# Kernel optimization log

Measured on AMD Instinct MI355X. Metric: run time of the kernel, lower is better.

The kernel has to match this reference:

```python
import jax, jax.numpy as jnp
import numpy as np

B, T, F_IN = 256, 168, 128
H = 512            # encoder hidden per direction; decoder hidden = 2H
OUT = 1
L_OUT = 48
SCALE = 0.05


def _lstm_scan(x, Wih, Whh, b, h0, c0):
    # x: [T, B, F]; PyTorch LSTM gate order i, f, g, o
    def step(carry, xt):
        h, c = carry
        g = xt @ Wih.T + h @ Whh.T + b
        i, f, gg, o = jnp.split(g, 4, axis=-1)
        c = jax.nn.sigmoid(f) * c + jax.nn.sigmoid(i) * jnp.tanh(gg)
        h = jax.nn.sigmoid(o) * jnp.tanh(c)
        return (h, c), h
    (hT, cT), ys = jax.lax.scan(step, (h0, c0), x)
    return ys, hT, cT


def setup_inputs() -> dict:
    key = jax.random.key(0)
    ks = jax.random.split(key, 16)
    r = lambda k, shp: (jax.random.normal(k, shp, dtype=jnp.float32) * SCALE)
    return {
        "input_seq": jax.random.normal(ks[0], (B, T, F_IN), dtype=jnp.float32),
        "enc_Wih_f": r(ks[1], (4 * H, F_IN)),
        "enc_Whh_f": r(ks[2], (4 * H, H)),
        "enc_bih_f": r(ks[3], (4 * H,)),
        "enc_bhh_f": r(ks[4], (4 * H,)),
        "enc_Wih_b": r(ks[5], (4 * H, F_IN)),
        "enc_Whh_b": r(ks[6], (4 * H, H)),
        "enc_bih_b": r(ks[7], (4 * H,)),
        "enc_bhh_b": r(ks[8], (4 * H,)),
        "dec_Wih": r(ks[9], (4 * 2 * H, OUT)),
        "dec_Whh": r(ks[10], (4 * 2 * H, 2 * H)),
        "dec_bih": r(ks[11], (4 * 2 * H,)),
        "dec_bhh": r(ks[12], (4 * 2 * H,)),
        "fc_W": r(ks[13], (OUT, 2 * H)),
        "fc_b": r(ks[14], (OUT,)),
        "output_length": L_OUT,
    }


def reference(input_seq, enc_Wih_f, enc_Whh_f, enc_bih_f, enc_bhh_f,
              enc_Wih_b, enc_Whh_b, enc_bih_b, enc_bhh_b,
              dec_Wih, dec_Whh, dec_bih, dec_bhh, fc_W, fc_b, output_length):
    b = input_seq.shape[0]
    h = enc_Whh_f.shape[1]
    x = jnp.transpose(input_seq, (1, 0, 2))  # [T, B, F]
    h0 = jnp.zeros((b, h), input_seq.dtype)
    c0 = jnp.zeros((b, h), input_seq.dtype)
    # bidirectional encoder (final hidden/cell only are used downstream)
    _, hf, cf = _lstm_scan(x, enc_Wih_f, enc_Whh_f, enc_bih_f + enc_bhh_f, h0, c0)
    _, hb, cb = _lstm_scan(x[::-1], enc_Wih_b, enc_Whh_b, enc_bih_b + enc_bhh_b, h0, c0)
    # _cat_hidden: concat fwd/bwd states along feature dim -> decoder init state [B, 2H]
    hd = jnp.concatenate([hf, hb], axis=-1)
    cd = jnp.concatenate([cf, cb], axis=-1)
    bd = dec_bih + dec_bhh
    x0 = jnp.zeros((b, fc_W.shape[0]), input_seq.dtype)  # initial decoder input = zeros

    def dec_step(carry, _):
        hh, cc, xt = carry
        g = xt @ dec_Wih.T + hh @ dec_Whh.T + bd
        i, f, gg, o = jnp.split(g, 4, axis=-1)
        cc = jax.nn.sigmoid(f) * cc + jax.nn.sigmoid(i) * jnp.tanh(gg)
        hh = jax.nn.sigmoid(o) * jnp.tanh(cc)
        pred = hh @ fc_W.T + fc_b  # [B, OUT]
        return (hh, cc, pred), pred

    _, preds = jax.lax.scan(dec_step, (hd, cd, x0), None, length=output_length)
    # [L, B, OUT] -> [B, L, OUT] -> squeeze(dim=2) with OUT==1 -> [B, L]
    return jnp.transpose(preds, (1, 0, 2)).squeeze(2)
```

## Files before the change

kernel.cpp:

```cpp
#include <hip/hip_runtime.h>


constexpr int B_ = 256, T_ = 168, F_ = 128, H_ = 512, L_ = 48;
constexpr int KE = F_ + H_;
constexpr int HD = 1024;
constexpr int GE = 4 * H_;
constexpr int EPAD = KE + 8;
constexpr int DPAD = HD + 8;

constexpr int FL256_IDX  = 0;
constexpr int CLAIM_IDX  = 256;
constexpr int ENCF_IDX   = 768;
constexpr int DECF_IDX   = 1280;
constexpr int CLAIM2_IDX = 2048;
constexpr int FL2_IDX    = 2560;

constexpr size_t OFF_SYNC = 0;
constexpr size_t OFF_WCF = 16384;
constexpr size_t OFF_WCB = OFF_WCF + (size_t)GE * KE * 2;
constexpr size_t OFF_PP  = OFF_WCB + (size_t)GE * KE * 2;
constexpr size_t OFF_BF  = OFF_PP  + (size_t)8 * 2 * 64 * 32 * 4;
constexpr size_t OFF_BB  = OFF_BF  + (size_t)GE * 4;
constexpr size_t OFF_XH  = OFF_BB  + (size_t)GE * 4;
constexpr size_t OFF_HE  = OFF_XH  + (size_t)T_ * B_ * F_ * 2;
constexpr size_t OFF_HDD = OFF_HE  + (size_t)2 * 2 * B_ * H_ * 2;
constexpr size_t OFF_CD  = OFF_HDD + (size_t)2 * B_ * HD * 2;

using h8 = __attribute__((ext_vector_type(8))) _Float16;
using f4 = __attribute__((ext_vector_type(4))) float;
using u4 = __attribute__((ext_vector_type(4))) unsigned;

#define DEV static __device__ __forceinline__

DEV float sigm(float x)  { return __fdividef(1.f, 1.f + __expf(-x)); }
DEV float tanh_(float x) { return 1.f - __fdividef(2.f, __expf(2.f * x) + 1.f); }

DEV h8 as_h8(f4 v) { union { f4 f; h8 h; } u; u.f = v; return u.h; }

DEV void astore_u64(void* p, unsigned long long v) {
  __hip_atomic_store((unsigned long long*)p, v, __ATOMIC_RELAXED,
                     __HIP_MEMORY_SCOPE_AGENT);
}
DEV void astore_u32(void* p, unsigned v) {
  __hip_atomic_store((unsigned*)p, v, __ATOMIC_RELAXED, __HIP_MEMORY_SCOPE_AGENT);
}
DEV unsigned aload_u32(const void* p) {
  return __hip_atomic_load((const unsigned*)p, __ATOMIC_RELAXED,
                           __HIP_MEMORY_SCOPE_AGENT);
}
DEV float aload_f32(const void* p) {
  return __hip_atomic_load((const float*)p, __ATOMIC_RELAXED,
                           __HIP_MEMORY_SCOPE_AGENT);
}
DEV void astore_f32(void* p, float v) {
  __hip_atomic_store((float*)p, v, __ATOMIC_RELAXED, __HIP_MEMORY_SCOPE_AGENT);
}
DEV void astore_u16(void* p, _Float16 v) {
  union { _Float16 h; unsigned short s; } u; u.h = v;
  __hip_atomic_store((unsigned short*)p, u.s, __ATOMIC_RELAXED,
                     __HIP_MEMORY_SCOPE_AGENT);
}
DEV void vm_drain() { asm volatile("s_waitcnt vmcnt(0)" ::: "memory"); }

template<bool DEEP>
DEV void ld16(const _Float16* p, f4* A) {
#define L16(FL) asm volatile( \
    "global_load_dwordx4 %0,  %16, off" FL "\n\t" \
    "global_load_dwordx4 %1,  %16, off offset:64" FL "\n\t" \
    "global_load_dwordx4 %2,  %16, off offset:128" FL "\n\t" \
    "global_load_dwordx4 %3,  %16, off offset:192" FL "\n\t" \
    "global_load_dwordx4 %4,  %16, off offset:256" FL "\n\t" \
    "global_load_dwordx4 %5,  %16, off offset:320" FL "\n\t" \
    "global_load_dwordx4 %6,  %16, off offset:384" FL "\n\t" \
    "global_load_dwordx4 %7,  %16, off offset:448" FL "\n\t" \
    "global_load_dwordx4 %8,  %16, off offset:512" FL "\n\t" \
    "global_load_dwordx4 %9,  %16, off offset:576" FL "\n\t" \
    "global_load_dwordx4 %10, %16, off offset:640" FL "\n\t" \
    "global_load_dwordx4 %11, %16, off offset:704" FL "\n\t" \
    "global_load_dwordx4 %12, %16, off offset:768" FL "\n\t" \
    "global_load_dwordx4 %13, %16, off offset:832" FL "\n\t" \
    "global_load_dwordx4 %14, %16, off offset:896" FL "\n\t" \
    "global_load_dwordx4 %15, %16, off offset:960" FL "\n\t" \
    "s_waitcnt vmcnt(0)" \
    : "=&v"(A[0]),"=&v"(A[1]),"=&v"(A[2]),"=&v"(A[3]),"=&v"(A[4]),"=&v"(A[5]), \
      "=&v"(A[6]),"=&v"(A[7]),"=&v"(A[8]),"=&v"(A[9]),"=&v"(A[10]),"=&v"(A[11]), \
      "=&v"(A[12]),"=&v"(A[13]),"=&v"(A[14]),"=&v"(A[15]) \
    : "v"(p) : "memory")
  if constexpr (DEEP) { L16(" sc0 sc1"); } else { L16(" sc0"); }
#undef L16
}

template<bool DEEP>
DEV void ld32(const _Float16* p, f4* A) {
#define L32(FL) asm volatile( \
    "global_load_dwordx4 %0,  %32, off" FL "\n\t" \
    "global_load_dwordx4 %1,  %32, off offset:64" FL "\n\t" \
    "global_load_dwordx4 %2,  %32, off offset:128" FL "\n\t" \
    "global_load_dwordx4 %3,  %32, off offset:192" FL "\n\t" \
    "global_load_dwordx4 %4,  %32, off offset:256" FL "\n\t" \
    "global_load_dwordx4 %5,  %32, off offset:320" FL "\n\t" \
    "global_load_dwordx4 %6,  %32, off offset:384" FL "\n\t" \
    "global_load_dwordx4 %7,  %32, off offset:448" FL "\n\t" \
    "global_load_dwordx4 %8,  %32, off offset:512" FL "\n\t" \
    "global_load_dwordx4 %9,  %32, off offset:576" FL "\n\t" \
    "global_load_dwordx4 %10, %32, off offset:640" FL "\n\t" \
    "global_load_dwordx4 %11, %32, off offset:704" FL "\n\t" \
    "global_load_dwordx4 %12, %32, off offset:768" FL "\n\t" \
    "global_load_dwordx4 %13, %32, off offset:832" FL "\n\t" \
    "global_load_dwordx4 %14, %32, off offset:896" FL "\n\t" \
    "global_load_dwordx4 %15, %32, off offset:960" FL "\n\t" \
    "global_load_dwordx4 %16, %32, off offset:1024" FL "\n\t" \
    "global_load_dwordx4 %17, %32, off offset:1088" FL "\n\t" \
    "global_load_dwordx4 %18, %32, off offset:1152" FL "\n\t" \
    "global_load_dwordx4 %19, %32, off offset:1216" FL "\n\t" \
    "global_load_dwordx4 %20, %32, off offset:1280" FL "\n\t" \
    "global_load_dwordx4 %21, %32, off offset:1344" FL "\n\t" \
    "global_load_dwordx4 %22, %32, off offset:1408" FL "\n\t" \
    "global_load_dwordx4 %23, %32, off offset:1472" FL "\n\t" \
    "global_load_dwordx4 %24, %32, off offset:1536" FL "\n\t" \
    "global_load_dwordx4 %25, %32, off offset:1600" FL "\n\t" \
    "global_load_dwordx4 %26, %32, off offset:1664" FL "\n\t" \
    "global_load_dwordx4 %27, %32, off offset:1728" FL "\n\t" \
    "global_load_dwordx4 %28, %32, off offset:1792" FL "\n\t" \
    "global_load_dwordx4 %29, %32, off offset:1856" FL "\n\t" \
    "global_load_dwordx4 %30, %32, off offset:1920" FL "\n\t" \
    "global_load_dwordx4 %31, %32, off offset:1984" FL "\n\t" \
    "s_waitcnt vmcnt(0)" \
    : "=&v"(A[0]),"=&v"(A[1]),"=&v"(A[2]),"=&v"(A[3]),"=&v"(A[4]),"=&v"(A[5]), \
      "=&v"(A[6]),"=&v"(A[7]),"=&v"(A[8]),"=&v"(A[9]),"=&v"(A[10]),"=&v"(A[11]), \
      "=&v"(A[12]),"=&v"(A[13]),"=&v"(A[14]),"=&v"(A[15]),"=&v"(A[16]),"=&v"(A[17]), \
      "=&v"(A[18]),"=&v"(A[19]),"=&v"(A[20]),"=&v"(A[21]),"=&v"(A[22]),"=&v"(A[23]), \
      "=&v"(A[24]),"=&v"(A[25]),"=&v"(A[26]),"=&v"(A[27]),"=&v"(A[28]),"=&v"(A[29]), \
      "=&v"(A[30]),"=&v"(A[31]) \
    : "v"(p) : "memory")
  if constexpr (DEEP) { L32(" sc0 sc1"); } else { L32(" sc0"); }
#undef L32
}

DEV void ld32s(const float* p, float* v) {
  asm volatile(
    "global_load_dword %0,  %32, off sc0 sc1\n\t"
    "global_load_dword %1,  %32, off offset:128 sc0 sc1\n\t"
    "global_load_dword %2,  %32, off offset:256 sc0 sc1\n\t"
    "global_load_dword %3,  %32, off offset:384 sc0 sc1\n\t"
    "global_load_dword %4,  %32, off offset:512 sc0 sc1\n\t"
    "global_load_dword %5,  %32, off offset:640 sc0 sc1\n\t"
    "global_load_dword %6,  %32, off offset:768 sc0 sc1\n\t"
    "global_load_dword %7,  %32, off offset:896 sc0 sc1\n\t"
    "global_load_dword %8,  %32, off offset:1024 sc0 sc1\n\t"
    "global_load_dword %9,  %32, off offset:1152 sc0 sc1\n\t"
    "global_load_dword %10, %32, off offset:1280 sc0 sc1\n\t"
    "global_load_dword %11, %32, off offset:1408 sc0 sc1\n\t"
    "global_load_dword %12, %32, off offset:1536 sc0 sc1\n\t"
    "global_load_dword %13, %32, off offset:1664 sc0 sc1\n\t"
    "global_load_dword %14, %32, off offset:1792 sc0 sc1\n\t"
    "global_load_dword %15, %32, off offset:1920 sc0 sc1\n\t"
    "global_load_dword %16, %32, off offset:2048 sc0 sc1\n\t"
    "global_load_dword %17, %32, off offset:2176 sc0 sc1\n\t"
    "global_load_dword %18, %32, off offset:2304 sc0 sc1\n\t"
    "global_load_dword %19, %32, off offset:2432 sc0 sc1\n\t"
    "global_load_dword %20, %32, off offset:2560 sc0 sc1\n\t"
    "global_load_dword %21, %32, off offset:2688 sc0 sc1\n\t"
    "global_load_dword %22, %32, off offset:2816 sc0 sc1\n\t"
    "global_load_dword %23, %32, off offset:2944 sc0 sc1\n\t"
    "global_load_dword %24, %32, off offset:3072 sc0 sc1\n\t"
    "global_load_dword %25, %32, off offset:3200 sc0 sc1\n\t"
    "global_load_dword %26, %32, off offset:3328 sc0 sc1\n\t"
    "global_load_dword %27, %32, off offset:3456 sc0 sc1\n\t"
    "global_load_dword %28, %32, off offset:3584 sc0 sc1\n\t"
    "global_load_dword %29, %32, off offset:3712 sc0 sc1\n\t"
    "global_load_dword %30, %32, off offset:3840 sc0 sc1\n\t"
    "global_load_dword %31, %32, off offset:3968 sc0 sc1\n\t"
    "s_waitcnt vmcnt(0)"
    : "=&v"(v[0]),"=&v"(v[1]),"=&v"(v[2]),"=&v"(v[3]),"=&v"(v[4]),"=&v"(v[5]),
      "=&v"(v[6]),"=&v"(v[7]),"=&v"(v[8]),"=&v"(v[9]),"=&v"(v[10]),"=&v"(v[11]),
      "=&v"(v[12]),"=&v"(v[13]),"=&v"(v[14]),"=&v"(v[15]),"=&v"(v[16]),"=&v"(v[17]),
      "=&v"(v[18]),"=&v"(v[19]),"=&v"(v[20]),"=&v"(v[21]),"=&v"(v[22]),"=&v"(v[23]),
      "=&v"(v[24]),"=&v"(v[25]),"=&v"(v[26]),"=&v"(v[27]),"=&v"(v[28]),"=&v"(v[29]),
      "=&v"(v[30]),"=&v"(v[31])
    : "v"(p) : "memory");
}

DEV unsigned pollflag(const unsigned* p, bool deep) {
  unsigned v;
  if (deep)
    asm volatile("global_load_dword %0, %1, off sc0 sc1\n\t"
                 "s_waitcnt vmcnt(0)" : "=&v"(v) : "v"(p) : "memory");
  else
    asm volatile("global_load_dword %0, %1, off sc0\n\t"
                 "s_waitcnt vmcnt(0)" : "=&v"(v) : "v"(p) : "memory");
  return v;
}
DEV void wait_ge(const unsigned* p, unsigned target, bool deep, int cap) {
  for (int it = 0; it < cap; ++it) {
    unsigned v = pollflag(p, deep);
    if (__ballot(v >= target) == ~0ull) return;
  }
}

DEV void gsync(unsigned* fl, int bi, unsigned phase, int tid) {
  vm_drain();
  __syncthreads();
  if (tid == 0) astore_u32(fl + bi, phase);
  if (tid < 64) {
    const unsigned* p = fl + tid * 4;
    for (int it = 0; it < (1 << 20); ++it) {
      u4 v;
      asm volatile("global_load_dwordx4 %0, %1, off sc0 sc1\n\t"
                   "s_waitcnt vmcnt(0)" : "=&v"(v) : "v"(p) : "memory");
      unsigned a = v[0] < v[1] ? v[0] : v[1];
      unsigned b = v[2] < v[3] ? v[2] : v[3];
      if (__ballot((a < b ? a : b) >= phase) == ~0ull) break;
    }
  }
  __syncthreads();
  asm volatile("" ::: "memory");
}

__global__ void prep_misc(const float* bihF, const float* bhhF,
                          const float* bihB, const float* bhhB, char* ws) {
  int i = blockIdx.x * blockDim.x + threadIdx.x;
  if (i < 2048) astore_u64(ws + (size_t)i * 8, 0ull);
  if (i < GE) {
    ((float*)(ws + OFF_BF))[i] = bihF[i] + bhhF[i];
    ((float*)(ws + OFF_BB))[i] = bihB[i] + bhhB[i];
  }
  if (i < 2 * 2 * B_ * H_ / 4) astore_u64((char*)ws + OFF_HE + (size_t)i * 8, 0ull);
}

__global__ void conv_encw(const float* WihF, const float* WhhF,
                          const float* WihB, const float* WhhB, char* ws) {
  int i = blockIdx.x * blockDim.x + threadIdx.x;
  if (i >= GE * KE) return;
  int r = i / KE, k = i - r * KE;
  float vF = (k < F_) ? WihF[r * F_ + k] : WhhF[r * H_ + (k - F_)];
  float vB = (k < F_) ? WihB[r * F_ + k] : WhhB[r * H_ + (k - F_)];
  ((_Float16*)(ws + OFF_WCF))[i] = (_Float16)vF;
  ((_Float16*)(ws + OFF_WCB))[i] = (_Float16)vB;
}

__global__ void conv_x(const float* x, char* ws) {
  int i = blockIdx.x * blockDim.x + threadIdx.x;
  if (i >= T_ * B_ * F_) return;
  int f = i & 127, b = (i >> 7) & 255, t = i >> 15;
  ((_Float16*)(ws + OFF_XH))[i] = (_Float16)x[((size_t)b * T_ + t) * F_ + f];
}

template<bool LOCAL>
DEV void encoder_phase(int dir, int chunk, int slice,
                       int tid, int wave, int quad, int col, int lane,
                       char* ws, _Float16* lds, _Float16 (*htile)[16]) {
  const _Float16* Wenc  = (const _Float16*)(ws + (dir ? OFF_WCB : OFF_WCF));
  const float*    biasE = (const float*)(ws + (dir ? OFF_BB : OFF_BF));
  const _Float16* Xh    = (const _Float16*)(ws + OFF_XH);
  _Float16* hE = (_Float16*)(ws + OFF_HE);
  _Float16* hD = (_Float16*)(ws + OFF_HDD);
  float*    cD = (float*)(ws + OFF_CD);
  unsigned* encf = (unsigned*)ws + ENCF_IDX + (dir * 4 + chunk) * 64;

  const int j0 = slice * 16;
  const int mb = chunk * 64;

  for (int it = 0; it < 20; ++it) {
    int idx = it * 256 + tid;
    int n = idx / 80, e = idx - n * 80;
    int g = n >> 4, u = n & 15;
    *((h8*)(lds + n * EPAD) + e) =
        *((const h8*)(Wenc + (size_t)(g * H_ + j0 + u) * KE) + e);
  }
  float breg[4];
#pragma unroll
  for (int g = 0; g < 4; ++g) breg[g] = biasE[g * H_ + j0 + col];
  float cst[4] = {0.f, 0.f, 0.f, 0.f};
  __syncthreads();

  h8 Bf[4][16];
#pragma unroll
  for (int g = 0; g < 4; ++g)
#pragma unroll
    for (int kk = 0; kk < 16; ++kk)
      Bf[g][kk] = *((const h8*)(lds + (g * 16 + col) * EPAD + F_) + kk * 4 + quad);

  const int arow = mb + wave * 16 + col;
  const int mrow = mb + wave * 16 + quad * 4;

  for (int t = 0; t < T_; ++t) {
    const int par = t & 1;
    const int tx  = dir ? (T_ - 1 - t) : t;
    f4 z = {0.f, 0.f, 0.f, 0.f};
    f4 acc[4] = {z, z, z, z};

    const h8* xr = (const h8*)(Xh + ((size_t)tx * B_ + arow) * F_);
#pragma unroll
    for (int kk = 0; kk < 4; ++kk) {
      h8 a = xr[kk * 4 + quad];
#pragma unroll
      for (int g = 0; g < 4; ++g) {
        h8 b = *((const h8*)(lds + (g * 16 + col) * EPAD) + kk * 4 + quad);
        acc[g] = __builtin_amdgcn_mfma_f32_16x16x32_f16(a, b, acc[g], 0, 0, 0);
      }
    }
    if (t > 0)
      wait_ge(encf + (lane & 31), (unsigned)t, !LOCAL, 1 << 16);
    f4 A[16];
    ld16<!LOCAL>(hE + ((size_t)(par * 2 + dir) * B_ + arow) * H_ + quad * 8, A);
#pragma unroll
    for (int kk = 0; kk < 16; ++kk) {
      h8 a = as_h8(A[kk]);
#pragma unroll
      for (int g = 0; g < 4; ++g)
        acc[g] = __builtin_amdgcn_mfma_f32_16x16x32_f16(a, Bf[g][kk], acc[g], 0, 0, 0);
    }

#pragma unroll
    for (int r = 0; r < 4; ++r) {
      float gi = acc[0][r] + breg[0];
      float gf = acc[1][r] + breg[1];
      float gg = acc[2][r] + breg[2];
      float go = acc[3][r] + breg[3];
      float c = sigm(gf) * cst[r] + sigm(gi) * tanh_(gg);
      cst[r] = c;
      float h = sigm(go) * tanh_(c);
      htile[wave * 16 + quad * 4 + r][col] = (_Float16)h;
      if (t == T_ - 1)
        astore_f32(&cD[(size_t)(mrow + r) * HD + dir * H_ + j0 + col], c);
    }
    __syncthreads();
    if (tid < 128) {
      int row = tid >> 1, half = tid & 1;
      const unsigned long long* src =
          (const unsigned long long*)&htile[row][half * 8];
      if (t < T_ - 1) {
        _Float16* dst = hE + ((size_t)((par ^ 1) * 2 + dir) * B_ + mb + row) * H_ +
                        j0 + half * 8;
        if (LOCAL) {
          ((unsigned long long*)dst)[0] = src[0];
          ((unsigned long long*)(dst + 4))[0] = src[1];
        } else {
          astore_u64(dst, src[0]);
          astore_u64(dst + 4, src[1]);
        }
      } else {
        _Float16* dst = hD + (size_t)(mb + row) * HD + dir * H_ + j0 + half * 8;
        astore_u64(dst, src[0]);
        astore_u64(dst + 4, src[1]);
      }
    }
    vm_drain();
    __syncthreads();
    if (tid == 0 && t < T_ - 1) {
      if (LOCAL) *(volatile unsigned*)(encf + slice) = (unsigned)(t + 1);
      else       astore_u32(encf + slice, (unsigned)(t + 1));
    }
  }
}

DEV void decoder_phase(int xcd, int rank, int tid, int wave, int quad, int col,
                       int lane, const float* dWih, const float* dWhh,
                       const float* dbih, const float* dbhh, const float* fcW,
                       const float* fcb, float* out, char* ws, _Float16* lds,
                       float* predbuf) {
  _Float16* hdd = (_Float16*)(ws + OFF_HDD);
  float* cD = (float*)(ws + OFF_CD);
  float* PP = (float*)(ws + OFF_PP) + (size_t)xcd * 2 * 64 * 32;
  unsigned* decf = (unsigned*)ws + DECF_IDX + xcd * 64;

  const int j0b = rank * 32;
  const int R0  = xcd * 32;
  const int m   = wave & 1;
  const int uh  = wave >> 1;
  const int unit = j0b + uh * 16 + col;
  const int arow = R0 + m * 16 + col;
  const int mrow = R0 + m * 16 + quad * 4;

  for (int it = 0; it < 64; ++it) {
    int idx = it * 256 + tid;
    int n = idx >> 8, c = idx & 255;
    int srow = (n >> 5) * HD + j0b + (n & 31);
    f4 w = *((const f4*)(dWhh + (size_t)srow * HD + c * 4));
    union { _Float16 h[4]; unsigned long long q; } u2;
#pragma unroll
    for (int i2 = 0; i2 < 4; ++i2) u2.h[i2] = (_Float16)w[i2];
    *(unsigned long long*)(lds + n * DPAD + c * 4) = u2.q;
  }
  h8 Bf[2][32];
#pragma unroll
  for (int gg = 0; gg < 2; ++gg)
#pragma unroll
    for (int kk = 0; kk < 32; ++kk) {
      const float* src = dWhh + (size_t)((2 + gg) * HD + unit) * HD + kk * 32 + quad * 8;
      f4 w0 = *((const f4*)src);
      f4 w1 = *((const f4*)(src + 4));
      union { _Float16 h[8]; h8 v; } u3;
#pragma unroll
      for (int i2 = 0; i2 < 4; ++i2) {
        u3.h[i2]     = (_Float16)w0[i2];
        u3.h[4 + i2] = (_Float16)w1[i2];
      }
      Bf[gg][kk] = u3.v;
    }
  float breg[4], wreg[4];
#pragma unroll
  for (int g = 0; g < 4; ++g) {
    breg[g] = dbih[g * HD + unit] + dbhh[g * HD + unit];
    wreg[g] = dWih[g * HD + unit];
  }
  const float fcw = fcW[unit];
  const float fb  = fcb[0];
  float cst[4];
#pragma unroll
  for (int r = 0; r < 4; ++r)
    cst[r] = aload_f32(cD + (size_t)(mrow + r) * HD + unit);
  __syncthreads();

  for (int l = 0; l <= L_; ++l) {
    float predv = 0.f;
    if (l > 0) {
      wait_ge(decf + (lane & 31), (unsigned)l, true, 1 << 16);
      const float* PPr = PP + (size_t)((l - 1) & 1) * 64 * 32;
      int row = lane & 31, halfsel = lane >> 5;
      const float* pb = PPr + (size_t)(halfsel * 32) * 32 + row;
      float pv[32], s = 0.f;
      ld32s(pb, pv);
#pragma unroll
      for (int j = 0; j < 32; ++j) s += pv[j];
      s += __shfl_xor(s, 32);
      predv = s + fb;
      if (rank == 0 && wave == 0 && lane < 32)
        predbuf[(l - 1) * 32 + lane] = predv;
    }
    if (l == L_) break;
    const int par = l & 1;

    f4 A[32];
    ld32<true>(hdd + ((size_t)par * B_ + arow) * HD + quad * 8, A);

    f4 z = {0.f, 0.f, 0.f, 0.f};
    f4 acc[4] = {z, z, z, z};
#pragma unroll
    for (int kk = 0; kk < 32; ++kk) {
      h8 a = as_h8(A[kk]);
      h8 b0 = *((const h8*)(lds + (0 * 32 + uh * 16 + col) * DPAD) + kk * 4 + quad);
      h8 b1 = *((const h8*)(lds + (1 * 32 + uh * 16 + col) * DPAD) + kk * 4 + quad);
      acc[0] = __builtin_amdgcn_mfma_f32_16x16x32_f16(a, b0, acc[0], 0, 0, 0);
      acc[1] = __builtin_amdgcn_mfma_f32_16x16x32_f16(a, b1, acc[1], 0, 0, 0);
      acc[2] = __builtin_amdgcn_mfma_f32_16x16x32_f16(a, Bf[0][kk], acc[2], 0, 0, 0);
      acc[3] = __builtin_amdgcn_mfma_f32_16x16x32_f16(a, Bf[1][kk], acc[3], 0, 0, 0);
    }

    float pr[4], sum[4];
#pragma unroll
    for (int r = 0; r < 4; ++r)
      pr[r] = (l > 0) ? __shfl(predv, m * 16 + quad * 4 + r) : 0.f;
#pragma unroll
    for (int r = 0; r < 4; ++r) {
      float gi = acc[0][r] + breg[0] + pr[r] * wreg[0];
      float gf = acc[1][r] + breg[1] + pr[r] * wreg[1];
      float gg = acc[2][r] + breg[2] + pr[r] * wreg[2];
      float go = acc[3][r] + breg[3] + pr[r] * wreg[3];
      float c = sigm(gf) * cst[r] + sigm(gi) * tanh_(gg);
      cst[r] = c;
      float h = sigm(go) * tanh_(c);
      size_t hoff = ((size_t)(par ^ 1) * B_ + mrow + r) * HD + unit;
      astore_u16(hdd + hoff, (_Float16)h);
      sum[r] = h * fcw;
    }
#pragma unroll
    for (int off = 1; off < 16; off <<= 1) {
#pragma unroll
      for (int r = 0; r < 4; ++r) sum[r] += __shfl_xor(sum[r], off, 16);
    }
    if (col == 0) {
      float* PPw = PP + (size_t)(l & 1) * 64 * 32;
      float* pdst = PPw + (size_t)(rank * 2 + uh) * 32 + m * 16 + quad * 4;
      union { float f[4]; unsigned long long q[2]; } u5;
#pragma unroll
      for (int r = 0; r < 4; ++r) u5.f[r] = sum[r];
      astore_u64(pdst, u5.q[0]);
      astore_u64(pdst + 2, u5.q[1]);
    }
    vm_drain();
    __syncthreads();
    if (tid == 0) astore_u32(decf + rank, (unsigned)(l + 1));
  }

  if (rank == 0) {
    __syncthreads();
    for (int idx = tid; idx < L_ * 32; idx += 256) {
      int row2 = idx & 31, st = idx >> 5;
      out[(size_t)(R0 + row2) * L_ + st] = predbuf[st * 32 + row2];
    }
  }
}

__global__ __launch_bounds__(256, 1)
void enc_kernel(char* __restrict__ ws) {
  __shared__ __align__(16) _Float16 lds[64 * EPAD];
  __shared__ __align__(16) _Float16 htile[64][16];
  __shared__ int sh[2];

  const int tid  = threadIdx.x;
  const int wave = tid >> 6;
  const int lane = tid & 63;
  const int quad = lane >> 4;
  const int col  = lane & 15;
  const int bi   = blockIdx.x;

  unsigned* sync  = (unsigned*)(ws + OFF_SYNC);
  unsigned* fl    = sync + FL256_IDX;
  unsigned* claim = sync + CLAIM_IDX;

  if (tid == 0) {
    unsigned x;
    asm volatile("s_getreg_b32 %0, hwreg(HW_REG_XCC_ID)" : "=s"(x));
    int xcd = (int)(x & 7u);
    unsigned r = __hip_atomic_fetch_add(claim + xcd * 64, 1u, __ATOMIC_RELAXED,
                                        __HIP_MEMORY_SCOPE_AGENT);
    sh[0] = xcd;
    sh[1] = (int)r;
  }
  __syncthreads();
  const int xcd = sh[0], rank = sh[1];
  gsync(fl, bi, 1u, tid);
  if (tid == 0) {
    int d = 0;
    for (int k = 0; k < 8; ++k)
      if (aload_u32(claim + k * 64) != 32u) d = 1;
    sh[0] = d;
  }
  __syncthreads();
  const bool deg = (sh[0] != 0) || (rank >= 32);

  if (!deg)
    encoder_phase<true>(xcd >> 2, xcd & 3, rank, tid, wave, quad, col, lane,
                        ws, lds, htile);
  else
    encoder_phase<false>(bi >> 7, bi & 3, (bi & 127) >> 2, tid, wave, quad, col,
                         lane, ws, lds, htile);
}

__global__ __launch_bounds__(256, 1)
void dec_kernel(const float* __restrict__ dWih, const float* __restrict__ dWhh,
                const float* __restrict__ dbih, const float* __restrict__ dbhh,
                const float* __restrict__ fcW, const float* __restrict__ fcb,
                float* __restrict__ out, char* __restrict__ ws) {
  __shared__ __align__(16) _Float16 lds[64 * DPAD];
  __shared__ __align__(16) float predbuf[L_ * 32];
  __shared__ int sh[2];

  const int tid  = threadIdx.x;
  const int wave = tid >> 6;
  const int lane = tid & 63;
  const int quad = lane >> 4;
  const int col  = lane & 15;
  const int bi   = blockIdx.x;

  unsigned* sync  = (unsigned*)(ws + OFF_SYNC);
  unsigned* fl2   = sync + FL2_IDX;
  unsigned* claim = sync + CLAIM2_IDX;

  if (tid == 0) {
    unsigned x;
    asm volatile("s_getreg_b32 %0, hwreg(HW_REG_XCC_ID)" : "=s"(x));
    int xcd = (int)(x & 7u);
    unsigned r = __hip_atomic_fetch_add(claim + xcd * 64, 1u, __ATOMIC_RELAXED,
                                        __HIP_MEMORY_SCOPE_AGENT);
    sh[0] = xcd;
    sh[1] = (int)r;
  }
  __syncthreads();
  const int xcd = sh[0], rank = sh[1];
  gsync(fl2, bi, 1u, tid);
  if (tid == 0) {
    int d = 0;
    for (int k = 0; k < 8; ++k)
      if (aload_u32(claim + k * 64) != 32u) d = 1;
    sh[0] = d;
  }
  __syncthreads();
  const bool deg = (sh[0] != 0) || (rank >= 32);

  if (!deg)
    decoder_phase(xcd, rank, tid, wave, quad, col, lane, dWih, dWhh,
                  dbih, dbhh, fcW, fcb, out, ws, lds, predbuf);
  else
    decoder_phase(bi >> 5, bi & 31, tid, wave, quad, col, lane, dWih,
                  dWhh, dbih, dbhh, fcW, fcb, out, ws, lds, predbuf);
}

extern "C" void kernel_launch(void* const* d_in, const int* in_sizes, int n_in,
                              void* d_out, int out_size, void* d_ws, size_t ws_size,
                              hipStream_t stream) {
  const float* x     = (const float*)d_in[0];
  const float* eWihF = (const float*)d_in[1];
  const float* eWhhF = (const float*)d_in[2];
  const float* ebihF = (const float*)d_in[3];
  const float* ebhhF = (const float*)d_in[4];
  const float* eWihB = (const float*)d_in[5];
  const float* eWhhB = (const float*)d_in[6];
  const float* ebihB = (const float*)d_in[7];
  const float* ebhhB = (const float*)d_in[8];
  const float* dWih  = (const float*)d_in[9];
  const float* dWhh  = (const float*)d_in[10];
  const float* dbih  = (const float*)d_in[11];
  const float* dbhh  = (const float*)d_in[12];
  const float* fcW   = (const float*)d_in[13];
  const float* fcb   = (const float*)d_in[14];
  float* out = (float*)d_out;
  char*  ws  = (char*)d_ws;

  prep_misc<<<512, 256, 0, stream>>>(ebihF, ebhhF, ebihB, ebhhB, ws);
  conv_encw<<<(GE * KE) / 256, 256, 0, stream>>>(eWihF, eWhhF, eWihB, eWhhB, ws);
  conv_x<<<(T_ * B_ * F_) / 256, 256, 0, stream>>>(x, ws);

  enc_kernel<<<dim3(256), dim3(256), 0, stream>>>(ws);
  dec_kernel<<<dim3(256), dim3(256), 0, stream>>>(dWih, dWhh, dbih, dbhh,
                                                  fcW, fcb, out, ws);
}
```

Baseline: 1.445 ms.

## Retile encoder blocks to 16 batch rows by 64 hidden units

```diff
diff --git a/kernel.cpp b/kernel.cpp
--- a/kernel.cpp
+++ b/kernel.cpp
@@ -5,15 +5,15 @@
 constexpr int KE = F_ + H_;
 constexpr int HD = 1024;
 constexpr int GE = 4 * H_;
-constexpr int EPAD = KE + 8;
+constexpr int XPAD = 136;
 constexpr int DPAD = HD + 8;
 
 constexpr int FL256_IDX  = 0;
 constexpr int CLAIM_IDX  = 256;
 constexpr int ENCF_IDX   = 768;
-constexpr int DECF_IDX   = 1280;
-constexpr int CLAIM2_IDX = 2048;
-constexpr int FL2_IDX    = 2560;
+constexpr int DECF_IDX   = 2816;
+constexpr int CLAIM2_IDX = 3328;
+constexpr int FL2_IDX    = 3840;
 
 constexpr size_t OFF_SYNC = 0;
 constexpr size_t OFF_WCF = 16384;
@@ -249,40 +249,41 @@
 template<bool LOCAL>
 DEV void encoder_phase(int dir, int chunk, int slice,
                        int tid, int wave, int quad, int col, int lane,
-                       char* ws, _Float16* lds, _Float16 (*htile)[16]) {
+                       char* ws, _Float16* xlds, _Float16 (*htile)[64]) {
   const _Float16* Wenc  = (const _Float16*)(ws + (dir ? OFF_WCB : OFF_WCF));
   const float*    biasE = (const float*)(ws + (dir ? OFF_BB : OFF_BF));
   const _Float16* Xh    = (const _Float16*)(ws + OFF_XH);
   _Float16* hE = (_Float16*)(ws + OFF_HE);
   _Float16* hD = (_Float16*)(ws + OFF_HDD);
   float*    cD = (float*)(ws + OFF_CD);
-  unsigned* encf = (unsigned*)ws + ENCF_IDX + (dir * 4 + chunk) * 64;
-
-  const int j0 = slice * 16;
-  const int mb = chunk * 64;
-
-  for (int it = 0; it < 20; ++it) {
+  unsigned* encf = (unsigned*)ws + ENCF_IDX + (dir * 16 + chunk) * 64;
+
+  const int j0 = slice * 64;
+  const int mb = chunk * 16;
+
+  for (int it = 0; it < 16; ++it) {
     int idx = it * 256 + tid;
-    int n = idx / 80, e = idx - n * 80;
-    int g = n >> 4, u = n & 15;
-    *((h8*)(lds + n * EPAD) + e) =
+    int n = idx >> 4, e = idx & 15;
+    int g = n >> 6, u = n & 63;
+    *((h8*)(xlds + (size_t)n * XPAD) + e) =
         *((const h8*)(Wenc + (size_t)(g * H_ + j0 + u) * KE) + e);
   }
+  const int unit = j0 + wave * 16 + col;
+  h8 Bf[4][16];
+#pragma unroll
+  for (int g = 0; g < 4; ++g)
+#pragma unroll
+    for (int kk = 0; kk < 16; ++kk)
+      Bf[g][kk] = *((const h8*)(Wenc + (size_t)(g * H_ + unit) * KE + F_) +
+                    kk * 4 + quad);
   float breg[4];
 #pragma unroll
-  for (int g = 0; g < 4; ++g) breg[g] = biasE[g * H_ + j0 + col];
+  for (int g = 0; g < 4; ++g) breg[g] = biasE[g * H_ + unit];
   float cst[4] = {0.f, 0.f, 0.f, 0.f};
   __syncthreads();
 
-  h8 Bf[4][16];
-#pragma unroll
-  for (int g = 0; g < 4; ++g)
-#pragma unroll
-    for (int kk = 0; kk < 16; ++kk)
-      Bf[g][kk] = *((const h8*)(lds + (g * 16 + col) * EPAD + F_) + kk * 4 + quad);
-
-  const int arow = mb + wave * 16 + col;
-  const int mrow = mb + wave * 16 + quad * 4;
+  const int arow  = mb + col;
+  const int mrowq = mb + quad * 4;
 
   for (int t = 0; t < T_; ++t) {
     const int par = t & 1;
@@ -296,12 +297,13 @@
       h8 a = xr[kk * 4 + quad];
 #pragma unroll
       for (int g = 0; g < 4; ++g) {
-        h8 b = *((const h8*)(lds + (g * 16 + col) * EPAD) + kk * 4 + quad);
+        h8 b = *((const h8*)(xlds + (size_t)(g * 64 + wave * 16 + col) * XPAD) +
+                 kk * 4 + quad);
         acc[g] = __builtin_amdgcn_mfma_f32_16x16x32_f16(a, b, acc[g], 0, 0, 0);
       }
     }
     if (t > 0)
-      wait_ge(encf + (lane & 31), (unsigned)t, !LOCAL, 1 << 16);
+      wait_ge(encf + (lane & 7), (unsigned)t, !LOCAL, 1 << 16);
     f4 A[16];
     ld16<!LOCAL>(hE + ((size_t)(par * 2 + dir) * B_ + arow) * H_ + quad * 8, A);
 #pragma unroll
@@ -321,18 +323,18 @@
       float c = sigm(gf) * cst[r] + sigm(gi) * tanh_(gg);
       cst[r] = c;
       float h = sigm(go) * tanh_(c);
-      htile[wave * 16 + quad * 4 + r][col] = (_Float16)h;
+      htile[quad * 4 + r][wave * 16 + col] = (_Float16)h;
       if (t == T_ - 1)
-        astore_f32(&cD[(size_t)(mrow + r) * HD + dir * H_ + j0 + col], c);
+        astore_f32(&cD[(size_t)(mrowq + r) * HD + dir * H_ + unit], c);
     }
     __syncthreads();
     if (tid < 128) {
-      int row = tid >> 1, half = tid & 1;
+      int row = tid >> 3, seg = tid & 7;
       const unsigned long long* src =
-          (const unsigned long long*)&htile[row][half * 8];
+          (const unsigned long long*)&htile[row][seg * 8];
       if (t < T_ - 1) {
         _Float16* dst = hE + ((size_t)((par ^ 1) * 2 + dir) * B_ + mb + row) * H_ +
-                        j0 + half * 8;
+                        j0 + seg * 8;
         if (LOCAL) {
           ((unsigned long long*)dst)[0] = src[0];
           ((unsigned long long*)(dst + 4))[0] = src[1];
@@ -341,7 +343,7 @@
           astore_u64(dst + 4, src[1]);
         }
       } else {
-        _Float16* dst = hD + (size_t)(mb + row) * HD + dir * H_ + j0 + half * 8;
+        _Float16* dst = hD + (size_t)(mb + row) * HD + dir * H_ + j0 + seg * 8;
         astore_u64(dst, src[0]);
         astore_u64(dst + 4, src[1]);
       }
@@ -495,8 +497,8 @@
 
 __global__ __launch_bounds__(256, 1)
 void enc_kernel(char* __restrict__ ws) {
-  __shared__ __align__(16) _Float16 lds[64 * EPAD];
-  __shared__ __align__(16) _Float16 htile[64][16];
+  __shared__ __align__(16) _Float16 xlds[256 * XPAD];
+  __shared__ __align__(16) _Float16 htile[16][64];
   __shared__ int sh[2];
 
   const int tid  = threadIdx.x;
@@ -531,12 +533,14 @@
   __syncthreads();
   const bool deg = (sh[0] != 0) || (rank >= 32);
 
-  if (!deg)
-    encoder_phase<true>(xcd >> 2, xcd & 3, rank, tid, wave, quad, col, lane,
-                        ws, lds, htile);
-  else
-    encoder_phase<false>(bi >> 7, bi & 3, (bi & 127) >> 2, tid, wave, quad, col,
-                         lane, ws, lds, htile);
+  if (!deg) {
+    encoder_phase<true>(xcd >> 2, (xcd & 3) * 4 + (rank >> 3), rank & 7,
+                        tid, wave, quad, col, lane, ws, xlds, htile);
+  } else {
+    int d2 = bi >> 7, rest = bi & 127;
+    encoder_phase<false>(d2, rest >> 3, rest & 7,
+                         tid, wave, quad, col, lane, ws, xlds, htile);
+  }
 }
 
 __global__ __launch_bounds__(256, 1)
```

Measured after the change: 1.415 ms. 2.1% less time.
